# Kernel tuning notes

Hardware: AMD Instinct MI355X
Metric: run time of the kernel (lower is better)

Reference implementation:

```python
import jax, jax.numpy as jnp
import numpy as np

B, L, D = 2, 2048, 1024
H = 16
HD = D // H  # 64


def setup_inputs() -> dict:
    key = jax.random.key(0)
    ks = jax.random.split(key, 7)
    s = 0.02
    return {
        "x": jax.random.normal(ks[0], (B, L, D), dtype=jnp.float32),
        "Wq": jax.random.normal(ks[1], (D, D), dtype=jnp.float32) * s,
        "bq": jnp.zeros((D,), dtype=jnp.float32),
        "Wkv": jax.random.normal(ks[2], (D, 2 * D), dtype=jnp.float32) * s,
        "bkv": jnp.zeros((2 * D,), dtype=jnp.float32),
        "Wo": jax.random.normal(ks[3], (D, D), dtype=jnp.float32) * s,
        "bo": jnp.zeros((D,), dtype=jnp.float32),
    }


def reference(x, Wq, bq, Wkv, bkv, Wo, bo):
    # q/kv projections (self-attention: key/value come from x)
    q = x @ Wq + bq                      # [B, L, D]
    kv = x @ Wkv + bkv                   # [B, L, 2D]
    k, v = jnp.split(kv, 2, axis=-1)     # each [B, L, D]
    # split heads: 'b l (h c) -> b h l c' (rope_embed_fraction=0 -> RoPE is identity)
    def heads(t):
        return t.reshape(B, L, H, HD).transpose(0, 2, 1, 3)
    qh, kh, vh = heads(q), heads(k), heads(v)   # [B, H, L, HD]
    scale = 1.0 / jnp.sqrt(jnp.asarray(HD, dtype=x.dtype))
    scores = jnp.einsum('bhqc,bhkc->bhqk', qh, kh) * scale  # [B, H, L, L]
    attn = jax.nn.softmax(scores, axis=-1)
    y = jnp.einsum('bhqk,bhkc->bhqc', attn, vh)             # [B, H, L, HD]
    # merge heads: 'b h l c -> b l (h c)'
    y = y.transpose(0, 2, 1, 3).reshape(B, L, D)
    return (y @ Wo + bo).reshape(x.shape)
```

## Files before the change

kernel.cpp:

```cpp
#include <hip/hip_runtime.h>

#define B_  2
#define L_  2048
#define D_  1024
#define H_  16
#define HD_ 64

typedef __attribute__((ext_vector_type(8))) short bf16x8;
typedef __attribute__((ext_vector_type(4))) float f32x4;

#define MFMA16(a, b, c) __builtin_amdgcn_mfma_f32_16x16x32_bf16(a, b, c, 0, 0, 0)

__device__ __forceinline__ unsigned short f2bf(float f) {
    union { float f; unsigned u; } v; v.f = f;
    unsigned r = v.u + 0x7FFFu + ((v.u >> 16) & 1u);
    return (unsigned short)(r >> 16);
}

__global__ __launch_bounds__(256) void prep_all(
    const float* __restrict__ x,
    const float* __restrict__ Wq, const float* __restrict__ Wkv,
    const float* __restrict__ Wo,
    unsigned short* __restrict__ xb,
    unsigned short* __restrict__ Wqt, unsigned short* __restrict__ Wkvt,
    unsigned short* __restrict__ Wot)
{
    const int z = blockIdx.z;
    if (z == 4) {
        const int bidl = blockIdx.y * 32 + blockIdx.x;
        const int n4 = B_ * L_ * D_ / 4;
        for (int i = bidl * 256 + threadIdx.x; i < n4; i += 1024 * 256) {
            float4 v = *(const float4*)(x + (size_t)i * 4);
            ushort4 u;
            u.x = f2bf(v.x); u.y = f2bf(v.y); u.z = f2bf(v.z); u.w = f2bf(v.w);
            *(ushort4*)(xb + (size_t)i * 4) = u;
        }
        return;
    }
    __shared__ float t[32][33];
    const float* W;  unsigned short* Wt;  int N, nc;
    if (z == 0)      { W = Wq;  Wt = Wqt;  N = 1024; nc = 0; }
    else if (z == 1) { W = Wo;  Wt = Wot;  N = 1024; nc = 0; }
    else             { W = Wkv; Wt = Wkvt; N = 2048; nc = (z - 2) * 1024; }
    const int tx = threadIdx.x & 31, ty = threadIdx.x >> 5;
    const int n0 = nc + blockIdx.x * 32, k0 = blockIdx.y * 32;
    #pragma unroll
    for (int r = 0; r < 4; ++r)
        t[ty + r * 8][tx] = W[(size_t)(k0 + ty + r * 8) * N + n0 + tx];
    __syncthreads();
    #pragma unroll
    for (int r = 0; r < 4; ++r)
        Wt[(size_t)(n0 + ty + r * 8) * 1024 + k0 + tx] = f2bf(t[tx][ty + r * 8]);
}

__global__ __launch_bounds__(512, 1) void gemm_qkv8(
    const unsigned short* __restrict__ A,
    const unsigned short* __restrict__ Bt,
    const float* __restrict__ bq, const float* __restrict__ bkv,
    unsigned short* __restrict__ Qb, unsigned short* __restrict__ Kb,
    unsigned short* __restrict__ Vtg, float qscl)
{
    const int KDIM = 1024, NT = 16;
    __shared__ __align__(16) unsigned short lds[65536];

    const int tid = threadIdx.x;
    const int w = tid >> 6, l = tid & 63, g = l >> 4, ln = l & 15;
    const int wm = (w >> 2) & 1, wn = w & 3;

    const int lin = blockIdx.x;
    const int wg = (lin & 7) * 24 + (lin >> 3);
    const int by = wg / 12, bx = wg % 12;
    const int m0 = by * 256, n0 = bx * 256;

    const int sr8 = w * 8 + (l >> 3);
    const int sc  = (l & 7) ^ ((l >> 3) & 7);
    const unsigned short* Asrc = A  + (size_t)m0 * KDIM + sc * 8;
    const unsigned short* Bsrc = Bt + (size_t)n0 * KDIM + sc * 8;

#define SLOT_A(d, h) (lds + ((d) * 2 + (h)) * 8192)
#define SLOT_B(d, h) (lds + 32768 + ((d) * 2 + (h)) * 8192)

#define STG(slotp, srcp, hh, kt_) do {                                        \
    _Pragma("unroll")                                                         \
    for (int r_ = 0; r_ < 2; ++r_) {                                          \
        const int row_ = (hh) * 128 + r_ * 64 + sr8;                          \
        __builtin_amdgcn_global_load_lds(                                     \
            (const __attribute__((address_space(1))) void*)                   \
                ((srcp) + (size_t)row_ * KDIM + (kt_) * 64),                  \
            (__attribute__((address_space(3))) void*)                         \
                ((slotp) + r_ * 4096 + w * 512 + l * 8),                      \
            16, 0, 0);                                                        \
    }                                                                         \
} while (0)

    f32x4 acc[8][4];
    #pragma unroll
    for (int i = 0; i < 8; ++i)
        #pragma unroll
        for (int j = 0; j < 4; ++j) acc[i][j] = (f32x4){0.f, 0.f, 0.f, 0.f};

    bf16x8 aR[4][2], bB0[2][2], bB1[2][2];

    STG(SLOT_A(0, 0), Asrc, 0, 0);
    STG(SLOT_B(0, 1), Bsrc, 1, 0);
    STG(SLOT_A(0, 1), Asrc, 1, 0);
    STG(SLOT_B(0, 0), Bsrc, 0, 0);
    STG(SLOT_A(1, 0), Asrc, 0, 1);
    STG(SLOT_B(1, 1), Bsrc, 1, 1);

    #pragma unroll 1
    for (int kt = 0; kt < NT; ++kt) {
        const int cur = kt & 1, nxt = cur ^ 1;
        asm volatile("s_waitcnt vmcnt(4)" ::: "memory");
        __builtin_amdgcn_s_barrier();

        #pragma unroll
        for (int mi = 0; mi < 4; ++mi)
            #pragma unroll
            for (int kc = 0; kc < 2; ++kc) {
                const int rho = wm * 64 + mi * 16 + ln, c = kc * 4 + g;
                aR[mi][kc] = *(const bf16x8*)
                    (SLOT_A(cur, 0) + rho * 64 + ((c ^ (rho & 7)) * 8));
            }
        #pragma unroll
        for (int ni = 0; ni < 2; ++ni)
            #pragma unroll
            for (int kc = 0; kc < 2; ++kc) {
                const int rho = wn * 32 + ni * 16 + ln, c = kc * 4 + g;
                bB0[ni][kc] = *(const bf16x8*)
                    (SLOT_B(cur, 0) + rho * 64 + ((c ^ (rho & 7)) * 8));
            }
        if (kt + 1 < NT) STG(SLOT_A(nxt, 1), Asrc, 1, kt + 1);
        __builtin_amdgcn_s_barrier();
        asm volatile("s_waitcnt lgkmcnt(0)" ::: "memory");
        __builtin_amdgcn_s_setprio(1);
        #pragma unroll
        for (int mi = 0; mi < 4; ++mi)
            #pragma unroll
            for (int ni = 0; ni < 2; ++ni) {
                acc[mi][ni] = MFMA16(aR[mi][0], bB0[ni][0], acc[mi][ni]);
                acc[mi][ni] = MFMA16(aR[mi][1], bB0[ni][1], acc[mi][ni]);
            }
        __builtin_amdgcn_s_setprio(0);
        __builtin_amdgcn_s_barrier();

        #pragma unroll
        for (int ni = 0; ni < 2; ++ni)
            #pragma unroll
            for (int kc = 0; kc < 2; ++kc) {
                const int rho = wn * 32 + ni * 16 + ln, c = kc * 4 + g;
                bB1[ni][kc] = *(const bf16x8*)
                    (SLOT_B(cur, 1) + rho * 64 + ((c ^ (rho & 7)) * 8));
            }
        if (kt + 1 < NT) STG(SLOT_B(nxt, 0), Bsrc, 0, kt + 1);
        __builtin_amdgcn_s_barrier();
        asm volatile("s_waitcnt lgkmcnt(0)" ::: "memory");
        __builtin_amdgcn_s_setprio(1);
        #pragma unroll
        for (int mi = 0; mi < 4; ++mi)
            #pragma unroll
            for (int ni = 0; ni < 2; ++ni) {
                acc[mi][2 + ni] = MFMA16(aR[mi][0], bB1[ni][0], acc[mi][2 + ni]);
                acc[mi][2 + ni] = MFMA16(aR[mi][1], bB1[ni][1], acc[mi][2 + ni]);
            }
        __builtin_amdgcn_s_setprio(0);
        __builtin_amdgcn_s_barrier();

        #pragma unroll
        for (int mi = 0; mi < 4; ++mi)
            #pragma unroll
            for (int kc = 0; kc < 2; ++kc) {
                const int rho = wm * 64 + mi * 16 + ln, c = kc * 4 + g;
                aR[mi][kc] = *(const bf16x8*)
                    (SLOT_A(cur, 1) + rho * 64 + ((c ^ (rho & 7)) * 8));
            }
        if (kt + 2 < NT) STG(SLOT_A(cur, 0), Asrc, 0, kt + 2);
        __builtin_amdgcn_s_barrier();
        asm volatile("s_waitcnt lgkmcnt(0)" ::: "memory");
        __builtin_amdgcn_s_setprio(1);
        #pragma unroll
        for (int mi = 0; mi < 4; ++mi)
            #pragma unroll
            for (int ni = 0; ni < 2; ++ni) {
                acc[4 + mi][2 + ni] = MFMA16(aR[mi][0], bB1[ni][0], acc[4 + mi][2 + ni]);
                acc[4 + mi][2 + ni] = MFMA16(aR[mi][1], bB1[ni][1], acc[4 + mi][2 + ni]);
            }
        __builtin_amdgcn_s_setprio(0);
        __builtin_amdgcn_s_barrier();

        if (kt + 2 < NT) STG(SLOT_B(cur, 1), Bsrc, 1, kt + 2);
        __builtin_amdgcn_s_barrier();
        __builtin_amdgcn_s_setprio(1);
        #pragma unroll
        for (int mi = 0; mi < 4; ++mi)
            #pragma unroll
            for (int ni = 0; ni < 2; ++ni) {
                acc[4 + mi][ni] = MFMA16(aR[mi][0], bB0[ni][0], acc[4 + mi][ni]);
                acc[4 + mi][ni] = MFMA16(aR[mi][1], bB0[ni][1], acc[4 + mi][ni]);
            }
        __builtin_amdgcn_s_setprio(0);
        __builtin_amdgcn_s_barrier();
    }
#undef STG
#undef SLOT_A
#undef SLOT_B

    const int region = n0 >> 10;
    if (region == 2) {
        #pragma unroll
        for (int nh = 0; nh < 2; ++nh)
            #pragma unroll
            for (int ni = 0; ni < 2; ++ni) {
                const int d = n0 - 2048 + nh * 128 + wn * 32 + ni * 16 + ln;
                const float bv = bkv[1024 + d];
                #pragma unroll
                for (int mh = 0; mh < 2; ++mh)
                    #pragma unroll
                    for (int mi = 0; mi < 4; ++mi) {
                        const int tok = m0 + mh * 128 + wm * 64 + mi * 16 + g * 4;
                        const int bb = tok >> 11, t4 = tok & 2047;
                        const f32x4 av = acc[mh * 4 + mi][nh * 2 + ni];
                        ushort4 p4;
                        p4.x = f2bf(av[0] + bv); p4.y = f2bf(av[1] + bv);
                        p4.z = f2bf(av[2] + bv); p4.w = f2bf(av[3] + bv);
                        *(ushort4*)(Vtg + ((size_t)bb * 1024 + d) * 2048 + t4) = p4;
                    }
            }
    } else {
        const int isQ = (region == 0);
        const float osc = isQ ? qscl : 1.f;
        #pragma unroll
        for (int nh = 0; nh < 2; ++nh)
            #pragma unroll
            for (int ni = 0; ni < 2; ++ni) {
                const int col = n0 + nh * 128 + wn * 32 + ni * 16 + ln;
                const float bv = isQ ? bq[col] : bkv[col - 1024];
                const int ck = isQ ? col : col - 1024;
                #pragma unroll
                for (int mh = 0; mh < 2; ++mh)
                    #pragma unroll
                    for (int mi = 0; mi < 4; ++mi) {
                        const int row = m0 + mh * 128 + wm * 64 + mi * 16 + g * 4;
                        const f32x4 av = acc[mh * 4 + mi][nh * 2 + ni];
                        #pragma unroll
                        for (int r = 0; r < 4; ++r) {
                            const float vout = (av[r] + bv) * osc;
                            if (isQ)
                                Qb[(size_t)(row + r) * 1024 + ck] = f2bf(vout);
                            else
                                Kb[(size_t)(row + r) * 1024 + ck] = f2bf(vout);
                        }
                    }
            }
    }
}

__global__ __launch_bounds__(256) void gemm_bt2(
    const unsigned short* __restrict__ A,
    const unsigned short* __restrict__ Bt,
    const float* __restrict__ bias,
    float* __restrict__ Cout)
{
    const int N = 1024, K = 1024;
    __shared__ __align__(16) unsigned short As[128 * 32];
    __shared__ __align__(16) unsigned short Bs[64 * 32];
    const int tid = threadIdx.x;
    const int w = tid >> 6, l = tid & 63, g = l >> 4, ln = l & 15;
    const int wm = w >> 1, wn = w & 1;
    const int dd = blockIdx.x;
    const int bid = (dd & 7) * 64 + (dd >> 3);
    const int m0 = (bid >> 4) * 128, n0 = (bid & 15) * 64;

    f32x4 acc[4][2];
    #pragma unroll
    for (int i = 0; i < 4; ++i)
        #pragma unroll
        for (int j = 0; j < 2; ++j) acc[i][j] = (f32x4){0.f, 0.f, 0.f, 0.f};

    const char* Ab = (const char*)A;
    const char* Bb = (const char*)Bt;
    const size_t strideK = (size_t)K * 2;

    const int brow = tid >> 2, bcb = (tid & 3) * 16;

    for (int k0 = 0; k0 < K; k0 += 32) {
        #pragma unroll
        for (int i = 0; i < 2; ++i) {
            const int b = w * 2048 + i * 1024 + l * 16;
            const int row = b >> 6, cb = b & 63;
            __builtin_amdgcn_global_load_lds(
                (const __attribute__((address_space(1))) void*)
                    (Ab + (size_t)(m0 + row) * strideK + (size_t)k0 * 2 + cb),
                (__attribute__((address_space(3))) void*)
                    ((char*)As + w * 2048 + i * 1024),
                16, 0, 0);
        }
        __builtin_amdgcn_global_load_lds(
            (const __attribute__((address_space(1))) void*)
                (Bb + (size_t)(n0 + brow) * strideK + (size_t)k0 * 2 + bcb),
            (__attribute__((address_space(3))) void*)
                ((char*)Bs + tid * 16),
            16, 0, 0);
        __syncthreads();
        bf16x8 af[4], bfr[2];
        #pragma unroll
        for (int m = 0; m < 4; ++m)
            af[m] = *(const bf16x8*)(As + (wm * 64 + m * 16 + ln) * 32 + g * 8);
        #pragma unroll
        for (int n = 0; n < 2; ++n)
            bfr[n] = *(const bf16x8*)(Bs + (wn * 32 + n * 16 + ln) * 32 + g * 8);
        #pragma unroll
        for (int m = 0; m < 4; ++m)
            #pragma unroll
            for (int n = 0; n < 2; ++n)
                acc[m][n] = MFMA16(af[m], bfr[n], acc[m][n]);
        __syncthreads();
    }

    #pragma unroll
    for (int n = 0; n < 2; ++n) {
        const int col = n0 + wn * 32 + n * 16 + ln;
        const float bv = bias[col];
        #pragma unroll
        for (int m = 0; m < 4; ++m) {
            const int row = m0 + wm * 64 + m * 16 + g * 4;
            #pragma unroll
            for (int r = 0; r < 4; ++r)
                Cout[(size_t)(row + r) * N + col] = acc[m][n][r] + bv;
        }
    }
}

__global__ __launch_bounds__(256) void attn_mfma(
    const unsigned short* __restrict__ Qb,
    const unsigned short* __restrict__ Kb,
    const unsigned short* __restrict__ Vtg,
    unsigned short* __restrict__ Yb)
{
    __shared__ __align__(16) unsigned short Ks[2][64 * 64];
    __shared__ __align__(16) unsigned short Vs[2][64 * 64];
    __shared__ __align__(16) unsigned short Pl[4][32 * 64];

    const int tid = threadIdx.x;
    const int w = tid >> 6, l = tid & 63, g = l >> 4, ln = l & 15;
    const int dd = blockIdx.x;
    const int bid = (dd & 7) * 64 + (dd >> 3);
    const int qc = bid & 15, h = (bid >> 4) & 15, b = bid >> 8;
    const int qrow = b * L_ + qc * 128 + w * 32;

    const int sub = l >> 3;
    const int scc = (l & 7) ^ sub;
    const unsigned short* ksrc = Kb  + (size_t)(b * L_) * 1024 + h * HD_ + scc * 8;
    const unsigned short* vsrc = Vtg + (size_t)(b * D_ + h * HD_) * 2048 + scc * 8;

#define STAGE(jj, bb) do {                                                    \
    _Pragma("unroll")                                                         \
    for (int i_ = 0; i_ < 2; ++i_) {                                          \
        const int rowK = w * 16 + i_ * 8 + sub;                               \
        __builtin_amdgcn_global_load_lds(                                     \
            (const __attribute__((address_space(1))) void*)                   \
                (ksrc + (size_t)((jj) * 64 + rowK) * 1024),                   \
            (__attribute__((address_space(3))) void*)                         \
                (&Ks[bb][w * 1024 + i_ * 512]), 16, 0, 0);                    \
        __builtin_amdgcn_global_load_lds(                                     \
            (const __attribute__((address_space(1))) void*)                   \
                (vsrc + (size_t)rowK * 2048 + (jj) * 64),                     \
            (__attribute__((address_space(3))) void*)                         \
                (&Vs[bb][w * 1024 + i_ * 512]), 16, 0, 0);                    \
    }                                                                         \
} while (0)

    bf16x8 qa[2][2];
    #pragma unroll
    for (int qt = 0; qt < 2; ++qt)
        #pragma unroll
        for (int c = 0; c < 2; ++c)
            qa[qt][c] = *(const bf16x8*)
                (Qb + (size_t)(qrow + qt * 16 + ln) * D_ + h * HD_ + c * 32 + g * 8);

    f32x4 o[2][4], lacc[2];
    #pragma unroll
    for (int qt = 0; qt < 2; ++qt) {
        #pragma unroll
        for (int dt = 0; dt < 4; ++dt) o[qt][dt] = (f32x4){0.f, 0.f, 0.f, 0.f};
        lacc[qt] = (f32x4){0.f, 0.f, 0.f, 0.f};
    }
    const short one_s = (short)0x3F80;
    const bf16x8 ones = {one_s, one_s, one_s, one_s, one_s, one_s, one_s, one_s};

    unsigned short* Pw = &Pl[w][0];
    const int swzl = (ln & 7) << 3;
    const int swp  = (ln & 7) << 1;

#define ATT_BODY(BUF, TNEXT, NBUF, DOSTG) do {                                \
    if (DOSTG) STAGE(TNEXT, NBUF);                                            \
    const unsigned short* Kc = &Ks[BUF][0];                                   \
    const unsigned short* Vc = &Vs[BUF][0];                                   \
    bf16x8 kb[4][2];                                                          \
    _Pragma("unroll")                                                         \
    for (int kt = 0; kt < 4; ++kt)                                            \
        _Pragma("unroll")                                                     \
        for (int c = 0; c < 2; ++c)                                           \
            kb[kt][c] = *(const bf16x8*)                                      \
                (Kc + (kt * 16 + ln) * 64 + ((c * 32 + g * 8) ^ swzl));       \
    f32x4 s[2][4];                                                            \
    const f32x4 z = (f32x4){0.f, 0.f, 0.f, 0.f};                              \
    __builtin_amdgcn_s_setprio(1);                                            \
    _Pragma("unroll")                                                         \
    for (int qt = 0; qt < 2; ++qt)                                            \
        _Pragma("unroll")                                                     \
        for (int kt = 0; kt < 4; ++kt) {                                      \
            f32x4 t0 = MFMA16(kb[kt][0], qa[qt][0], z);                       \
            s[qt][kt] = MFMA16(kb[kt][1], qa[qt][1], t0);                     \
        }                                                                     \
    __builtin_amdgcn_s_setprio(0);                                            \
    _Pragma("unroll")                                                         \
    for (int qt = 0; qt < 2; ++qt) {                                          \
        const int prow = (qt * 16 + ln) * 64;                                 \
        _Pragma("unroll")                                                     \
        for (int kt = 0; kt < 4; ++kt) {                                      \
            union { float f; unsigned u; } c0, c1, c2u, c3;                   \
            c0.f = __builtin_exp2f(s[qt][kt][0]);                             \
            c1.f = __builtin_exp2f(s[qt][kt][1]);                             \
            c2u.f = __builtin_exp2f(s[qt][kt][2]);                            \
            c3.f = __builtin_exp2f(s[qt][kt][3]);                             \
            uint2 pk;                                                         \
            pk.x = __builtin_amdgcn_perm(c1.u, c0.u, 0x07060302u);            \
            pk.y = __builtin_amdgcn_perm(c3.u, c2u.u, 0x07060302u);           \
            *(uint2*)(Pw + prow + (((kt * 4 + g) ^ swp) << 2)) = pk;          \
        }                                                                     \
    }                                                                         \
    bf16x8 pa[2][2], vb[4][2];                                                \
    _Pragma("unroll")                                                         \
    for (int qt = 0; qt < 2; ++qt)                                            \
        _Pragma("unroll")                                                     \
        for (int c2 = 0; c2 < 2; ++c2)                                        \
            pa[qt][c2] = *(const bf16x8*)                                     \
                (Pw + (qt * 16 + ln) * 64 + (((c2 * 8 + g * 2) ^ swp) << 2)); \
    _Pragma("unroll")                                                         \
    for (int dt = 0; dt < 4; ++dt)                                            \
        _Pragma("unroll")                                                     \
        for (int c2 = 0; c2 < 2; ++c2)                                        \
            vb[dt][c2] = *(const bf16x8*)                                     \
                (Vc + (dt * 16 + ln) * 64 + ((c2 * 32 + g * 8) ^ swzl));      \
    __builtin_amdgcn_s_setprio(1);                                            \
    _Pragma("unroll")                                                         \
    for (int qt = 0; qt < 2; ++qt) {                                          \
        lacc[qt] = MFMA16(pa[qt][0], ones, lacc[qt]);                         \
        lacc[qt] = MFMA16(pa[qt][1], ones, lacc[qt]);                         \
        _Pragma("unroll")                                                     \
        for (int dt = 0; dt < 4; ++dt) {                                      \
            o[qt][dt] = MFMA16(pa[qt][0], vb[dt][0], o[qt][dt]);              \
            o[qt][dt] = MFMA16(pa[qt][1], vb[dt][1], o[qt][dt]);              \
        }                                                                     \
    }                                                                         \
    __builtin_amdgcn_s_setprio(0);                                            \
} while (0)

    STAGE(0, 0);
    __syncthreads();

    #pragma unroll 1
    for (int t = 0; t < L_ / 64; t += 2) {
        ATT_BODY(0, t + 1, 1, true);
        __syncthreads();
        ATT_BODY(1, t + 2, 0, (t + 2 < L_ / 64));
        __syncthreads();
    }
#undef ATT_BODY
#undef STAGE

    #pragma unroll
    for (int qt = 0; qt < 2; ++qt)
        #pragma unroll
        for (int r = 0; r < 4; ++r) {
            const float inv = 1.f / lacc[qt][r];
            const int row = qrow + qt * 16 + g * 4 + r;
            #pragma unroll
            for (int dt = 0; dt < 4; ++dt)
                Yb[(size_t)row * D_ + h * HD_ + dt * 16 + ln] =
                    f2bf(o[qt][dt][r] * inv);
        }
}

extern "C" void kernel_launch(void* const* d_in, const int* in_sizes, int n_in,
                              void* d_out, int out_size, void* d_ws, size_t ws_size,
                              hipStream_t stream)
{
    const float* x   = (const float*)d_in[0];
    const float* Wq  = (const float*)d_in[1];
    const float* bq  = (const float*)d_in[2];
    const float* Wkv = (const float*)d_in[3];
    const float* bkv = (const float*)d_in[4];
    const float* Wo  = (const float*)d_in[5];
    const float* bo  = (const float*)d_in[6];
    float* out = (float*)d_out;

    const int M = B_ * L_;
    unsigned short* ws = (unsigned short*)d_ws;
    unsigned short* xb   = ws;
    unsigned short* Wqt  = xb   + (size_t)M * D_;
    unsigned short* Wkvt = Wqt  + (size_t)D_ * D_;
    unsigned short* Wot  = Wkvt + (size_t)2 * D_ * D_;
    unsigned short* Qb   = Wot  + (size_t)D_ * D_;
    unsigned short* Kb   = Qb   + (size_t)M * D_;
    unsigned short* Vtg  = Kb   + (size_t)M * D_;
    unsigned short* Yb   = Vtg  + (size_t)B_ * D_ * L_;

    const float QSCL = 0.125f * 1.44269504089f;

    prep_all<<<dim3(32, 32, 5), 256, 0, stream>>>(
        x, Wq, Wkv, Wo, xb, Wqt, Wkvt, Wot);

    gemm_qkv8<<<dim3(192), 512, 0, stream>>>(xb, Wqt, bq, bkv, Qb, Kb, Vtg, QSCL);

    attn_mfma<<<dim3(B_ * H_ * (L_ / 128)), 256, 0, stream>>>(Qb, Kb, Vtg, Yb);

    gemm_bt2<<<dim3(512), 256, 0, stream>>>(Yb, Wot, bo, out);
}
```

Measured before the change: 131.1 us.

## Software-pipeline attention S/PV phases and widen GEMM K-tile with swizzled LDS

The attention kernel is split into S_CORE (QK^T, exp, P write) and O_PHASE (PV MFMAs). Tile t's PV is now interleaved with tile t+1's score computation, using double-buffered P scratch and V fragments held in registers, so exp work overlaps MFMA work. The output-projection GEMM moves from a K-tile of 32 to 64 with an XOR-swizzled LDS layout, which halves the barriers per K loop and aims to avoid bank conflicts. The attention kernel also gets launch_bounds(256,2). The extra live V registers and doubled P LDS could raise register pressure or limit occupancy.

After: 123.7 us. 1.06x faster.

```diff
diff --git a/kernel.cpp b/kernel.cpp
--- a/kernel.cpp
+++ b/kernel.cpp
@@ -262,8 +262,8 @@
     float* __restrict__ Cout)
 {
     const int N = 1024, K = 1024;
-    __shared__ __align__(16) unsigned short As[128 * 32];
-    __shared__ __align__(16) unsigned short Bs[64 * 32];
+    __shared__ __align__(16) unsigned short As[128 * 64];
+    __shared__ __align__(16) unsigned short Bs[64 * 64];
     const int tid = threadIdx.x;
     const int w = tid >> 6, l = tid & 63, g = l >> 4, ln = l & 15;
     const int wm = w >> 1, wn = w & 1;
@@ -271,49 +271,61 @@
     const int bid = (dd & 7) * 64 + (dd >> 3);
     const int m0 = (bid >> 4) * 128, n0 = (bid & 15) * 64;
 
+    const int sr8 = w * 8 + (l >> 3);
+    const int sc  = (l & 7) ^ ((l >> 3) & 7);
+    const unsigned short* Asrc = A  + (size_t)m0 * K + sc * 8;
+    const unsigned short* Bsrc = Bt + (size_t)n0 * K + sc * 8;
+
     f32x4 acc[4][2];
     #pragma unroll
     for (int i = 0; i < 4; ++i)
         #pragma unroll
         for (int j = 0; j < 2; ++j) acc[i][j] = (f32x4){0.f, 0.f, 0.f, 0.f};
 
-    const char* Ab = (const char*)A;
-    const char* Bb = (const char*)Bt;
-    const size_t strideK = (size_t)K * 2;
-
-    const int brow = tid >> 2, bcb = (tid & 3) * 16;
-
-    for (int k0 = 0; k0 < K; k0 += 32) {
-        #pragma unroll
-        for (int i = 0; i < 2; ++i) {
-            const int b = w * 2048 + i * 1024 + l * 16;
-            const int row = b >> 6, cb = b & 63;
+    for (int k0 = 0; k0 < K; k0 += 64) {
+        #pragma unroll
+        for (int r_ = 0; r_ < 4; ++r_)
             __builtin_amdgcn_global_load_lds(
                 (const __attribute__((address_space(1))) void*)
-                    (Ab + (size_t)(m0 + row) * strideK + (size_t)k0 * 2 + cb),
+                    (Asrc + (size_t)(r_ * 32 + sr8) * K + k0),
                 (__attribute__((address_space(3))) void*)
-                    ((char*)As + w * 2048 + i * 1024),
+                    (As + r_ * 2048 + w * 512 + l * 8),
                 16, 0, 0);
-        }
-        __builtin_amdgcn_global_load_lds(
-            (const __attribute__((address_space(1))) void*)
-                (Bb + (size_t)(n0 + brow) * strideK + (size_t)k0 * 2 + bcb),
-            (__attribute__((address_space(3))) void*)
-                ((char*)Bs + tid * 16),
-            16, 0, 0);
+        #pragma unroll
+        for (int r_ = 0; r_ < 2; ++r_)
+            __builtin_amdgcn_global_load_lds(
+                (const __attribute__((address_space(1))) void*)
+                    (Bsrc + (size_t)(r_ * 32 + sr8) * K + k0),
+                (__attribute__((address_space(3))) void*)
+                    (Bs + r_ * 2048 + w * 512 + l * 8),
+                16, 0, 0);
         __syncthreads();
-        bf16x8 af[4], bfr[2];
-        #pragma unroll
-        for (int m = 0; m < 4; ++m)
-            af[m] = *(const bf16x8*)(As + (wm * 64 + m * 16 + ln) * 32 + g * 8);
-        #pragma unroll
-        for (int n = 0; n < 2; ++n)
-            bfr[n] = *(const bf16x8*)(Bs + (wn * 32 + n * 16 + ln) * 32 + g * 8);
-        #pragma unroll
-        for (int m = 0; m < 4; ++m)
-            #pragma unroll
-            for (int n = 0; n < 2; ++n)
-                acc[m][n] = MFMA16(af[m], bfr[n], acc[m][n]);
+        bf16x8 af[4][2], bfr[2][2];
+        #pragma unroll
+        for (int mi = 0; mi < 4; ++mi)
+            #pragma unroll
+            for (int kc = 0; kc < 2; ++kc) {
+                const int rho = wm * 64 + mi * 16 + ln, c = kc * 4 + g;
+                af[mi][kc] = *(const bf16x8*)
+                    (As + rho * 64 + ((c ^ (rho & 7)) * 8));
+            }
+        #pragma unroll
+        for (int ni = 0; ni < 2; ++ni)
+            #pragma unroll
+            for (int kc = 0; kc < 2; ++kc) {
+                const int rho = wn * 32 + ni * 16 + ln, c = kc * 4 + g;
+                bfr[ni][kc] = *(const bf16x8*)
+                    (Bs + rho * 64 + ((c ^ (rho & 7)) * 8));
+            }
+        __builtin_amdgcn_s_setprio(1);
+        #pragma unroll
+        for (int mi = 0; mi < 4; ++mi)
+            #pragma unroll
+            for (int ni = 0; ni < 2; ++ni) {
+                acc[mi][ni] = MFMA16(af[mi][0], bfr[ni][0], acc[mi][ni]);
+                acc[mi][ni] = MFMA16(af[mi][1], bfr[ni][1], acc[mi][ni]);
+            }
+        __builtin_amdgcn_s_setprio(0);
         __syncthreads();
     }
 
@@ -331,7 +343,7 @@
     }
 }
 
-__global__ __launch_bounds__(256) void attn_mfma(
+__global__ __launch_bounds__(256, 2) void attn_mfma(
     const unsigned short* __restrict__ Qb,
     const unsigned short* __restrict__ Kb,
     const unsigned short* __restrict__ Vtg,
@@ -339,7 +351,7 @@
 {
     __shared__ __align__(16) unsigned short Ks[2][64 * 64];
     __shared__ __align__(16) unsigned short Vs[2][64 * 64];
-    __shared__ __align__(16) unsigned short Pl[4][32 * 64];
+    __shared__ __align__(16) unsigned short Pl[4][2][32 * 64];
 
     const int tid = threadIdx.x;
     const int w = tid >> 6, l = tid & 63, g = l >> 4, ln = l & 15;
@@ -388,12 +400,13 @@
     const short one_s = (short)0x3F80;
     const bf16x8 ones = {one_s, one_s, one_s, one_s, one_s, one_s, one_s, one_s};
 
-    unsigned short* Pw = &Pl[w][0];
+    unsigned short* Pw = &Pl[w][0][0];
     const int swzl = (ln & 7) << 3;
     const int swp  = (ln & 7) << 1;
 
-#define ATT_BODY(BUF, TNEXT, NBUF, DOSTG) do {                                \
-    if (DOSTG) STAGE(TNEXT, NBUF);                                            \
+    bf16x8 vbA[4][2], vbB[4][2];
+
+#define S_CORE(BUF, PWS, VARR) do {                                           \
     const unsigned short* Kc = &Ks[BUF][0];                                   \
     const unsigned short* Vc = &Vs[BUF][0];                                   \
     bf16x8 kb[4][2];                                                          \
@@ -414,6 +427,12 @@
             s[qt][kt] = MFMA16(kb[kt][1], qa[qt][1], t0);                     \
         }                                                                     \
     __builtin_amdgcn_s_setprio(0);                                            \
+    _Pragma("unroll")                                                         \
+    for (int dt = 0; dt < 4; ++dt)                                            \
+        _Pragma("unroll")                                                     \
+        for (int c2 = 0; c2 < 2; ++c2)                                        \
+            VARR[dt][c2] = *(const bf16x8*)                                   \
+                (Vc + (dt * 16 + ln) * 64 + ((c2 * 32 + g * 8) ^ swzl));      \
     _Pragma("unroll")                                                         \
     for (int qt = 0; qt < 2; ++qt) {                                          \
         const int prow = (qt * 16 + ln) * 64;                                 \
@@ -427,22 +446,21 @@
             uint2 pk;                                                         \
             pk.x = __builtin_amdgcn_perm(c1.u, c0.u, 0x07060302u);            \
             pk.y = __builtin_amdgcn_perm(c3.u, c2u.u, 0x07060302u);           \
-            *(uint2*)(Pw + prow + (((kt * 4 + g) ^ swp) << 2)) = pk;          \
+            *(uint2*)(Pw + (PWS) * 2048 + prow +                              \
+                      (((kt * 4 + g) ^ swp) << 2)) = pk;                      \
         }                                                                     \
     }                                                                         \
-    bf16x8 pa[2][2], vb[4][2];                                                \
+} while (0)
+
+#define O_PHASE(PPWS, PVARR) do {                                             \
+    bf16x8 pa[2][2];                                                          \
     _Pragma("unroll")                                                         \
     for (int qt = 0; qt < 2; ++qt)                                            \
         _Pragma("unroll")                                                     \
         for (int c2 = 0; c2 < 2; ++c2)                                        \
             pa[qt][c2] = *(const bf16x8*)                                     \
-                (Pw + (qt * 16 + ln) * 64 + (((c2 * 8 + g * 2) ^ swp) << 2)); \
-    _Pragma("unroll")                                                         \
-    for (int dt = 0; dt < 4; ++dt)                                            \
-        _Pragma("unroll")                                                     \
-        for (int c2 = 0; c2 < 2; ++c2)                                        \
-            vb[dt][c2] = *(const bf16x8*)                                     \
-                (Vc + (dt * 16 + ln) * 64 + ((c2 * 32 + g * 8) ^ swzl));      \
+                (Pw + (PPWS) * 2048 + (qt * 16 + ln) * 64 +                   \
+                 (((c2 * 8 + g * 2) ^ swp) << 2));                            \
     __builtin_amdgcn_s_setprio(1);                                            \
     _Pragma("unroll")                                                         \
     for (int qt = 0; qt < 2; ++qt) {                                          \
@@ -450,8 +468,8 @@
         lacc[qt] = MFMA16(pa[qt][1], ones, lacc[qt]);                         \
         _Pragma("unroll")                                                     \
         for (int dt = 0; dt < 4; ++dt) {                                      \
-            o[qt][dt] = MFMA16(pa[qt][0], vb[dt][0], o[qt][dt]);              \
-            o[qt][dt] = MFMA16(pa[qt][1], vb[dt][1], o[qt][dt]);              \
+            o[qt][dt] = MFMA16(pa[qt][0], PVARR[dt][0], o[qt][dt]);           \
+            o[qt][dt] = MFMA16(pa[qt][1], PVARR[dt][1], o[qt][dt]);           \
         }                                                                     \
     }                                                                         \
     __builtin_amdgcn_s_setprio(0);                                            \
@@ -460,14 +478,27 @@
     STAGE(0, 0);
     __syncthreads();
 
+    STAGE(1, 1);
+    S_CORE(0, 0, vbA);
+    __syncthreads();
+
     #pragma unroll 1
-    for (int t = 0; t < L_ / 64; t += 2) {
-        ATT_BODY(0, t + 1, 1, true);
+    for (int t = 1; t < 31; t += 2) {
+        STAGE(t + 1, 0);
+        O_PHASE(0, vbA);
+        S_CORE(1, 1, vbB);
         __syncthreads();
-        ATT_BODY(1, t + 2, 0, (t + 2 < L_ / 64));
+        if (t + 2 < 32) STAGE(t + 2, 1);
+        O_PHASE(1, vbB);
+        S_CORE(0, 0, vbA);
         __syncthreads();
     }
-#undef ATT_BODY
+
+    O_PHASE(0, vbA);
+    S_CORE(1, 1, vbB);
+    O_PHASE(1, vbB);
+#undef O_PHASE
+#undef S_CORE
 #undef STAGE
 
     #pragma unroll
```
